# Optimization experiments

Hardware: AMD Instinct MI355X
Metric: run time of the kernel (lower is better)

Reference implementation:

```python
import jax, jax.numpy as jnp
import numpy as np

B, C, IMG, P_SZ = 32, 3, 224, 16
NPATCH = (IMG // P_SZ) ** 2  # 196
D, H, LAYERS, MLP = 768, 12, 12, 3072
HD = D // H
POOL, SEL, PLEN, NCLS = 10, 5, 5, 100
LN_EPS = 1e-6


def layer_norm(x, w, b):
    m = jnp.mean(x, -1, keepdims=True)
    v = jnp.var(x, -1, keepdims=True)
    return (x - m) * jax.lax.rsqrt(v + LN_EPS) * w + b


def vit_blocks(x, stacked):
    def blk(x, p):
        l1w, l1b, qw, qb, pw, pb, l2w, l2b, f1w, f1b, f2w, f2b = p
        b, s, _ = x.shape
        h = layer_norm(x, l1w, l1b)
        qkv = (h @ qw + qb).reshape(b, s, 3, H, HD).transpose(2, 0, 3, 1, 4)
        q, k, v = qkv[0], qkv[1], qkv[2]
        att = jax.nn.softmax(jnp.einsum('bhqd,bhkd->bhqk', q, k) * (HD ** -0.5), axis=-1)
        o = jnp.einsum('bhqk,bhkd->bhqd', att, v).transpose(0, 2, 1, 3).reshape(b, s, D)
        x = x + o @ pw + pb
        h = layer_norm(x, l2w, l2b)
        x = x + jax.nn.gelu(h @ f1w + f1b, approximate=False) @ f2w + f2b
        return x, None
    return jax.lax.scan(blk, x, stacked)[0]


def forward(inputs, patch_w, patch_b, cls_token, pos_embed,
            ln1_w, ln1_b, qkv_w, qkv_b, proj_w, proj_b,
            ln2_w, ln2_b, fc1_w, fc1_b, fc2_w, fc2_b,
            norm_w, norm_b, head_w, head_b,
            key_pool, frequency, prompts, variance, inv_variance):
    b = inputs.shape[0]
    g = IMG // P_SZ
    # patchify: 16x16/s16 conv == linear over [C,ph,pw]-flattened patches
    patches = inputs.reshape(b, C, g, P_SZ, g, P_SZ).transpose(0, 2, 4, 1, 3, 5).reshape(b, NPATCH, C * P_SZ * P_SZ)
    x = patches @ patch_w + patch_b  # [B,196,D]
    t = jnp.concatenate([jnp.broadcast_to(cls_token, (b, 1, D)), x], axis=1)
    x = t + pos_embed  # [B,197,D]
    stacked = (ln1_w, ln1_b, qkv_w, qkv_b, proj_w, proj_b, ln2_w, ln2_b, fc1_w, fc1_b, fc2_w, fc2_b)
    q = vit_blocks(x, stacked)
    q = layer_norm(q, norm_w, norm_b)[:, 0]  # CLS query [B,D]
    # Mahalanobis routing. torch computes exp(-quad/2)*(2pi)^{D/2}*||var||_F^{1/2},
    # which overflows fp32; we rank in log-domain (monotone-identical, constant
    # (D/2)log(2pi) dropped), so topk indices match the intended math.
    diff = q[:, None, :] - jax.lax.stop_gradient(key_pool)  # [B,POOL,D]
    quad = jnp.einsum('bpd,pde,bpe->bp', diff, inv_variance, diff)
    lognorm = 0.5 * jnp.log(jnp.linalg.norm(variance.reshape(POOL, -1), axis=-1))
    logprob = -0.5 * quad + lognorm
    w = frequency.max() - frequency  # F.normalize(...)
    wn = w / jnp.maximum(jnp.linalg.norm(w), 1e-12)
    score = logprob + jnp.log(jnp.maximum(wn, 1e-30))
    _, topk = jax.lax.top_k(-score, SEL)  # smallest SEL, ascending by score
    p = prompts[topk].reshape(b, SEL * PLEN, D) + pos_embed[0, 0]
    sx = jnp.concatenate([x[:, :1], p, x[:, 1:]], axis=1)  # [B,222,D]
    sx = vit_blocks(sx, stacked)
    sx = layer_norm(sx, norm_w, norm_b)
    feat = sx[:, 1:SEL * PLEN + 1].mean(axis=1)
    return feat @ head_w + head_b


def setup_inputs():
    key = jax.random.key(0)
    ks = jax.random.split(key, 16)
    std = 0.02
    inp = {
        'inputs': jax.random.normal(ks[0], (B, C, IMG, IMG), jnp.float32),
        'patch_w': jax.random.normal(ks[1], (C * P_SZ * P_SZ, D)) * std,
        'patch_b': jnp.zeros((D,)),
        'cls_token': jax.random.normal(ks[2], (1, 1, D)) * std,
        'pos_embed': jax.random.normal(ks[3], (1, NPATCH + 1, D)) * std,
        'ln1_w': jnp.ones((LAYERS, D)), 'ln1_b': jnp.zeros((LAYERS, D)),
        'qkv_w': jax.random.normal(ks[4], (LAYERS, D, 3 * D)) * std,
        'qkv_b': jnp.zeros((LAYERS, 3 * D)),
        'proj_w': jax.random.normal(ks[5], (LAYERS, D, D)) * std,
        'proj_b': jnp.zeros((LAYERS, D)),
        'ln2_w': jnp.ones((LAYERS, D)), 'ln2_b': jnp.zeros((LAYERS, D)),
        'fc1_w': jax.random.normal(ks[6], (LAYERS, D, MLP)) * std,
        'fc1_b': jnp.zeros((LAYERS, MLP)),
        'fc2_w': jax.random.normal(ks[7], (LAYERS, MLP, D)) * std,
        'fc2_b': jnp.zeros((LAYERS, D)),
        'norm_w': jnp.ones((D,)), 'norm_b': jnp.zeros((D,)),
        'head_w': jax.random.normal(ks[8], (D, NCLS)) * std,
        'head_b': jnp.zeros((NCLS,)),
        'key_pool': jax.random.normal(ks[9], (POOL, D)),
        'frequency': jax.random.randint(ks[10], (POOL,), 1, 100).astype(jnp.float32),
        'prompts': jax.random.normal(ks[11], (POOL, PLEN, D)) * std,
    }
    a = jax.random.uniform(ks[12], (POOL, D, D)) * 2.0
    var = a + jnp.swapaxes(a, -1, -2)  # symmetric, as in __init__
    inp['variance'] = var
    inp['inv_variance'] = jnp.linalg.inv(var)
    return inp


reference = forward
```

## Files before the change

kernel.cpp:

```cpp
#include <hip/hip_runtime.h>
#include <math.h>

#define S_PAD  224
#define NTOK   7168
#define DM     768
#define NH     12
#define HDIM   64
#define DMLP   3072
#define NBATCH 32
#define NLAYER 12
#define NPOOL  10
#define NSEL   5
#define NPLEN  5
#define NCLS   100
#define LN_EPS 1e-6f

typedef _Float16 f16_t;
typedef _Float16 f16x8 __attribute__((ext_vector_type(8)));
typedef float    floatx4 __attribute__((ext_vector_type(4)));

__device__ inline void cp16_lds(void* lds, const void* gp) {
    __builtin_amdgcn_global_load_lds((const __attribute__((address_space(1))) void*)gp,
                                     (__attribute__((address_space(3))) void*)lds, 16, 0, 0);
}

__global__ void wconv_t(const float* __restrict__ W, f16_t* __restrict__ WT, int K, int N) {
    int layer = blockIdx.z;
    const float* Wp = W + (long)layer * K * N;
    f16_t* Tp = WT + (long)layer * K * N;
    __shared__ float tile[32][33];
    int n0 = blockIdx.x * 32, k0 = blockIdx.y * 32;
    int tc = threadIdx.x & 31, tr = threadIdx.x >> 5;
    #pragma unroll
    for (int rr = 0; rr < 32; rr += 8)
        tile[tr + rr][tc] = Wp[(long)(k0 + tr + rr) * N + n0 + tc];
    __syncthreads();
    #pragma unroll
    for (int rr = 0; rr < 32; rr += 8)
        Tp[(long)(n0 + tr + rr) * K + k0 + tc] = (f16_t)tile[tc][tr + rr];
}

__global__ void patchify(const float* __restrict__ inp, f16_t* __restrict__ PATCH) {
    int s = blockIdx.x, b = blockIdx.y, t = threadIdx.x;
    f16_t* dst = PATCH + ((long)b * S_PAD + s) * DM;
    if (s >= 196) { for (int e = t; e < DM; e += 256) dst[e] = (f16_t)0.0f; return; }
    int py = s / 14, px = s % 14;
    for (int e = t; e < DM; e += 256) {
        int c = e >> 8, ph = (e >> 4) & 15, pw = e & 15;
        dst[e] = (f16_t)inp[(((long)b * 3 + c) * 224 + py * 16 + ph) * 224 + px * 16 + pw];
    }
}

template<int EPI, int BM>
__global__ __launch_bounds__(256) void gemm_f16(
    const f16_t* __restrict__ A, const f16_t* __restrict__ Bt,
    const float* __restrict__ bias, const float* __restrict__ resid,
    float* __restrict__ outf, f16_t* __restrict__ outb, int N, int K)
{
    constexpr int MI = BM / 32;
    __shared__ __align__(16) f16_t ldsA[BM * 32];
    __shared__ __align__(16) f16_t ldsB[128 * 32];
    const int t = threadIdx.x;
    const int w = t >> 6, l = t & 63;
    const int lr = l & 15, quad = l >> 4;
    const long m0 = (long)blockIdx.x * BM, n0 = (long)blockIdx.y * 128;
    const int r = t >> 2, c8 = (t & 3) << 3;
    const f16_t* Ap = A + (m0 + (r % BM)) * (long)K + c8;
    const f16_t* Bp = Bt + (n0 + r) * (long)K + c8;
    const int wm = (w >> 1) * (BM >> 1), wn = (w & 1) << 6;
    char* lbA = (char*)ldsA + (w << 10);
    char* lbB = (char*)ldsB + (w << 10);
    floatx4 acc[MI][4];
    #pragma unroll
    for (int i = 0; i < MI; i++)
        #pragma unroll
        for (int j = 0; j < 4; j++) acc[i][j] = (floatx4){0.f, 0.f, 0.f, 0.f};

    for (int k0 = 0; k0 < K; k0 += 32) {
        __syncthreads();
        cp16_lds(lbA, Ap + k0);
        if (BM == 128) cp16_lds(lbA + 4096, Ap + (long)64 * K + k0);
        cp16_lds(lbB,        Bp + k0);
        cp16_lds(lbB + 4096, Bp + (long)64 * K + k0);
        __syncthreads();
        f16x8 af[MI], bf[4];
        #pragma unroll
        for (int mi = 0; mi < MI; mi++)
            af[mi] = *(const f16x8*)((const char*)ldsA + ((wm + mi * 16 + lr) << 6) + (quad << 4));
        #pragma unroll
        for (int ni = 0; ni < 4; ni++)
            bf[ni] = *(const f16x8*)((const char*)ldsB + ((wn + ni * 16 + lr) << 6) + (quad << 4));
        #pragma unroll
        for (int mi = 0; mi < MI; mi++)
            #pragma unroll
            for (int ni = 0; ni < 4; ni++)
                acc[mi][ni] = __builtin_amdgcn_mfma_f32_16x16x32_f16(af[mi], bf[ni], acc[mi][ni], 0, 0, 0);
    }
    #pragma unroll
    for (int mi = 0; mi < MI; mi++) {
        const long row = m0 + wm + mi * 16 + quad * 4;
        #pragma unroll
        for (int ni = 0; ni < 4; ni++) {
            const long col = n0 + wn + ni * 16 + lr;
            const float bv = bias[col];
            #pragma unroll
            for (int rg = 0; rg < 4; rg++) {
                long idx = (row + rg) * (long)N + col;
                float v = acc[mi][ni][rg] + bv;
                if (EPI == 0) outf[idx] = v;
                else if (EPI == 1) outb[idx] = (f16_t)v;
                else if (EPI == 2) outf[idx] = v + resid[idx];
                else {
                    v = 0.5f * v * (1.0f + erff(v * 0.70710678118654752f));
                    outb[idx] = (f16_t)v;
                }
            }
        }
    }
}

__global__ void assemble_x0(const float* __restrict__ PE, const float* __restrict__ cls,
                            const float* __restrict__ pos, float* __restrict__ X0,
                            float* __restrict__ X) {
    int s = blockIdx.x, b = blockIdx.y, t = threadIdx.x;
    long o = ((long)b * S_PAD + s) * DM;
    for (int e = t; e < DM; e += 256) {
        float v;
        if (s == 0)        v = cls[e] + pos[e];
        else if (s <= 196) v = PE[((long)b * S_PAD + (s - 1)) * DM + e] + pos[(long)s * DM + e];
        else               v = 0.0f;
        X0[o + e] = v; X[o + e] = v;
    }
}

__global__ __launch_bounds__(256) void ln_to_f16(const float* __restrict__ X,
        const float* __restrict__ gw, const float* __restrict__ gb, f16_t* __restrict__ out) {
    const long row = blockIdx.x;
    const int t = threadIdx.x;
    const float* x = X + row * DM;
    float v0 = x[t], v1 = x[t + 256], v2 = x[t + 512];
    float s = v0 + v1 + v2, ss = v0 * v0 + v1 * v1 + v2 * v2;
    #pragma unroll
    for (int off = 32; off; off >>= 1) { s += __shfl_down(s, off); ss += __shfl_down(ss, off); }
    __shared__ float sa[8];
    int w = t >> 6;
    if ((t & 63) == 0) { sa[w] = s; sa[4 + w] = ss; }
    __syncthreads();
    s = sa[0] + sa[1] + sa[2] + sa[3]; ss = sa[4] + sa[5] + sa[6] + sa[7];
    float mean = s * (1.0f / DM);
    float var = ss * (1.0f / DM) - mean * mean;
    float rs = rsqrtf(var + LN_EPS);
    f16_t* o = out + row * DM;
    o[t]       = (f16_t)((v0 - mean) * rs * gw[t]       + gb[t]);
    o[t + 256] = (f16_t)((v1 - mean) * rs * gw[t + 256] + gb[t + 256]);
    o[t + 512] = (f16_t)((v2 - mean) * rs * gw[t + 512] + gb[t + 512]);
}

__global__ __launch_bounds__(256) void v_trans(const f16_t* __restrict__ qkv,
                                               f16_t* __restrict__ vtg) {
    int bh = blockIdx.x, b = bh / NH, h = bh % NH;
    __shared__ __align__(16) char lds[32768];
    int t = threadIdx.x, w = t >> 6, l = t & 63;
    const f16_t* Vb = qkv + (long)b * S_PAD * 2304 + 1536 + h * HDIM;
    #pragma unroll
    for (int q = 0; q < 8; q++) {
        int c0 = q * 256 + w * 64;
        int cc = c0 + l;
        int j = cc / 9, part = cc - j * 9;
        if (j > 223) j = 223;
        if (part > 7) part = 7;
        cp16_lds(lds + (size_t)c0 * 16, Vb + (long)j * 2304 + part * 8);
    }
    __syncthreads();
    const f16_t* Vs = (const f16_t*)lds;
    f16_t* dst = vtg + (long)bh * HDIM * S_PAD;
    #pragma unroll
    for (int it = 0; it < 56; it++) {
        int e = it * 256 + t;
        int d = e / S_PAD, j = e - d * S_PAD;
        dst[e] = Vs[j * 72 + d];
    }
}

__global__ __launch_bounds__(256) void attn_fused(const f16_t* __restrict__ qkv,
        const f16_t* __restrict__ vtg, f16_t* __restrict__ AO, int S) {
    int bh = blockIdx.y, b = bh / NH, h = bh % NH;
    int i0 = blockIdx.x * 64;
    int t = threadIdx.x, w = t >> 6, l = t & 63;
    int lr = l & 15, quad = l >> 4;
    __shared__ __align__(16) char lds[62464];
    const f16_t* Kb = qkv + (long)b * S_PAD * 2304 + 768 + h * HDIM;
    const f16_t* Qb = qkv + (long)b * S_PAD * 2304 + h * HDIM;
    const f16_t* Vg = vtg + (long)bh * HDIM * S_PAD;

    #pragma unroll
    for (int q = 0; q < 8; q++) {
        int c0 = q * 256 + w * 64;
        int cc = c0 + l;
        int j = cc / 9, part = cc - j * 9;
        if (j > 223) j = 223;
        if (part > 7) part = 7;
        cp16_lds(lds + (size_t)c0 * 16, Kb + (long)j * 2304 + part * 8);
    }
    #pragma unroll
    for (int q = 0; q < 8; q++) {
        int c0 = q * 256 + w * 64;
        if (c0 < 1856) {
            int cc = c0 + l;
            int d = cc / 29, part = cc - d * 29;
            if (part > 27) part = 27;
            cp16_lds(lds + 32768 + (size_t)c0 * 16, Vg + (long)d * S_PAD + part * 8);
        }
    }
    int qr = i0 + w * 16 + lr;
    if (qr > S_PAD - 1) qr = S_PAD - 1;
    long qrow = (long)qr * 2304;
    f16x8 qf0 = *(const f16x8*)(Qb + qrow + quad * 8);
    f16x8 qf1 = *(const f16x8*)(Qb + qrow + 32 + quad * 8);
    __syncthreads();

    const f16_t* Ks = (const f16_t*)lds;
    floatx4 acc[14];
    #pragma unroll
    for (int jt = 0; jt < 14; jt++) {
        floatx4 a = (floatx4){0.f, 0.f, 0.f, 0.f};
        f16x8 k0 = *(const f16x8*)(Ks + (jt * 16 + lr) * 72 + quad * 8);
        f16x8 k1 = *(const f16x8*)(Ks + (jt * 16 + lr) * 72 + 32 + quad * 8);
        a = __builtin_amdgcn_mfma_f32_16x16x32_f16(qf0, k0, a, 0, 0, 0);
        a = __builtin_amdgcn_mfma_f32_16x16x32_f16(qf1, k1, a, 0, 0, 0);
        acc[jt] = a;
    }
    float mx[4] = {-3.0e38f, -3.0e38f, -3.0e38f, -3.0e38f};
    #pragma unroll
    for (int jt = 0; jt < 14; jt++) {
        bool valid = (jt * 16 + lr) < S;
        #pragma unroll
        for (int rg = 0; rg < 4; rg++) {
            float v = valid ? acc[jt][rg] * 0.125f : -3.0e38f;
            acc[jt][rg] = v;
            mx[rg] = fmaxf(mx[rg], v);
        }
    }
    #pragma unroll
    for (int rg = 0; rg < 4; rg++)
        #pragma unroll
        for (int m = 1; m < 16; m <<= 1) mx[rg] = fmaxf(mx[rg], __shfl_xor(mx[rg], m));
    float sm[4] = {0.f, 0.f, 0.f, 0.f};
    #pragma unroll
    for (int jt = 0; jt < 14; jt++)
        #pragma unroll
        for (int rg = 0; rg < 4; rg++) {
            float e = __expf(acc[jt][rg] - mx[rg]);
            acc[jt][rg] = e; sm[rg] += e;
        }
    #pragma unroll
    for (int rg = 0; rg < 4; rg++)
        #pragma unroll
        for (int m = 1; m < 16; m <<= 1) sm[rg] += __shfl_xor(sm[rg], m);

    __syncthreads();
    f16_t* Pw = (f16_t*)lds + w * 16 * 232;
    #pragma unroll
    for (int jt = 0; jt < 14; jt++)
        #pragma unroll
        for (int rg = 0; rg < 4; rg++)
            Pw[(quad * 4 + rg) * 232 + jt * 16 + lr] = (f16_t)acc[jt][rg];

    const f16_t* Vt = (const f16_t*)(lds + 32768);
    floatx4 oacc[4];
    #pragma unroll
    for (int dt = 0; dt < 4; dt++) oacc[dt] = (floatx4){0.f, 0.f, 0.f, 0.f};
    #pragma unroll
    for (int ks = 0; ks < 7; ks++) {
        f16x8 a = *(const f16x8*)(Pw + lr * 232 + ks * 32 + quad * 8);
        #pragma unroll
        for (int dt = 0; dt < 4; dt++) {
            f16x8 bb = *(const f16x8*)(Vt + (dt * 16 + lr) * 232 + ks * 32 + quad * 8);
            oacc[dt] = __builtin_amdgcn_mfma_f32_16x16x32_f16(a, bb, oacc[dt], 0, 0, 0);
        }
    }
    if (i0 + w * 16 < S_PAD) {
        float inv[4];
        #pragma unroll
        for (int rg = 0; rg < 4; rg++) inv[rg] = 1.0f / sm[rg];
        f16_t* dst = AO + (long)b * S_PAD * DM + h * HDIM;
        #pragma unroll
        for (int dt = 0; dt < 4; dt++)
            #pragma unroll
            for (int rg = 0; rg < 4; rg++)
                dst[(long)(i0 + w * 16 + quad * 4 + rg) * DM + dt * 16 + lr] = (f16_t)(oacc[dt][rg] * inv[rg]);
    }
}

__global__ void cls_ln(const float* __restrict__ X, const float* __restrict__ gw,
                       const float* __restrict__ gb, float* __restrict__ q) {
    int b = blockIdx.x, t = threadIdx.x;
    const float* x = X + (long)b * S_PAD * DM;
    float v0 = x[t], v1 = x[t + 256], v2 = x[t + 512];
    float s = v0 + v1 + v2, ss = v0 * v0 + v1 * v1 + v2 * v2;
    #pragma unroll
    for (int off = 32; off; off >>= 1) { s += __shfl_down(s, off); ss += __shfl_down(ss, off); }
    __shared__ float sa[8];
    int w = t >> 6;
    if ((t & 63) == 0) { sa[w] = s; sa[4 + w] = ss; }
    __syncthreads();
    s = sa[0] + sa[1] + sa[2] + sa[3]; ss = sa[4] + sa[5] + sa[6] + sa[7];
    float mean = s * (1.0f / DM);
    float rs = rsqrtf(ss * (1.0f / DM) - mean * mean + LN_EPS);
    q[(long)b * DM + t]       = (v0 - mean) * rs * gw[t]       + gb[t];
    q[(long)b * DM + t + 256] = (v1 - mean) * rs * gw[t + 256] + gb[t + 256];
    q[(long)b * DM + t + 512] = (v2 - mean) * rs * gw[t + 512] + gb[t + 512];
}

__global__ void var_ssq(const float* __restrict__ var, float* __restrict__ ssq) {
    int p = blockIdx.x, chunk = blockIdx.y;
    const float* v = var + (long)p * DM * DM + (long)chunk * 16384;
    float s = 0.f;
    for (int i = threadIdx.x; i < 16384; i += 256) { float x = v[i]; s += x * x; }
    #pragma unroll
    for (int off = 32; off; off >>= 1) s += __shfl_down(s, off);
    __shared__ float sa[4];
    int w = threadIdx.x >> 6;
    if ((threadIdx.x & 63) == 0) sa[w] = s;
    __syncthreads();
    if (threadIdx.x == 0) atomicAdd(&ssq[p], sa[0] + sa[1] + sa[2] + sa[3]);
}

__global__ void route_coef(const float* __restrict__ ssq, const float* __restrict__ freq,
                           float* __restrict__ coef) {
    if (threadIdx.x == 0) {
        float fm = freq[0];
        for (int p = 1; p < NPOOL; p++) fm = fmaxf(fm, freq[p]);
        float w[NPOOL]; float n2 = 0.f;
        for (int p = 0; p < NPOOL; p++) { w[p] = fm - freq[p]; n2 += w[p] * w[p]; }
        float nrm = fmaxf(sqrtf(n2), 1e-12f);
        for (int p = 0; p < NPOOL; p++) {
            float wn = w[p] / nrm;
            coef[p] = 0.25f * logf(ssq[p]) + logf(fmaxf(wn, 1e-30f));
        }
    }
}

__global__ __launch_bounds__(256) void route_quad(const float* __restrict__ q,
        const float* __restrict__ kp, const float* __restrict__ iv,
        const float* __restrict__ coef, float* __restrict__ score) {
    int b = blockIdx.x, p = blockIdx.y, t = threadIdx.x;
    __shared__ float diff[DM];
    for (int e = t; e < DM; e += 256) diff[e] = q[(long)b * DM + e] - kp[(long)p * DM + e];
    __syncthreads();
    const float* M = iv + (long)p * DM * DM;
    float u0 = 0.f, u1 = 0.f, u2 = 0.f;
    for (int i = 0; i < DM; i++) {
        float di = diff[i];
        const float* r = M + (long)i * DM;
        u0 += di * r[t]; u1 += di * r[t + 256]; u2 += di * r[t + 512];
    }
    float part = u0 * diff[t] + u1 * diff[t + 256] + u2 * diff[t + 512];
    #pragma unroll
    for (int off = 32; off; off >>= 1) part += __shfl_down(part, off);
    __shared__ float sa[4];
    if ((t & 63) == 0) sa[t >> 6] = part;
    __syncthreads();
    if (t == 0) score[b * NPOOL + p] = -0.5f * (sa[0] + sa[1] + sa[2] + sa[3]) + coef[p];
}

__global__ void topk_kernel(const float* __restrict__ score, int* __restrict__ topk) {
    int b = threadIdx.x;
    if (b < NBATCH) {
        float s[NPOOL]; bool used[NPOOL];
        for (int p = 0; p < NPOOL; p++) { s[p] = score[b * NPOOL + p]; used[p] = false; }
        for (int k = 0; k < NSEL; k++) {
            int best = 0; float bv = 3.4e38f;
            for (int p = 0; p < NPOOL; p++)
                if (!used[p] && s[p] < bv) { bv = s[p]; best = p; }
            used[best] = true; topk[b * NSEL + k] = best;
        }
    }
}

__global__ void assemble_sx(const float* __restrict__ X0, const float* __restrict__ prompts,
                            const float* __restrict__ pos, const int* __restrict__ topk,
                            float* __restrict__ X) {
    int s = blockIdx.x, b = blockIdx.y, t = threadIdx.x;
    long o = ((long)b * S_PAD + s) * DM;
    for (int e = t; e < DM; e += 256) {
        float v;
        if (s == 0) v = X0[(long)b * S_PAD * DM + e];
        else if (s <= 25) {
            int j = s - 1;
            int pr = topk[b * NSEL + j / NPLEN];
            v = prompts[((long)pr * NPLEN + j % NPLEN) * DM + e] + pos[e];
        } else if (s <= 221) {
            v = X0[((long)b * S_PAD + (s - 25)) * DM + e];
        } else v = 0.0f;
        X[o + e] = v;
    }
}

__global__ __launch_bounds__(256) void feat_ln_mean(const float* __restrict__ X,
        const float* __restrict__ gw, const float* __restrict__ gb, float* __restrict__ feat) {
    int b = blockIdx.x, t = threadIdx.x;
    __shared__ float sa[8];
    float f0 = 0.f, f1 = 0.f, f2 = 0.f;
    for (int j = 1; j <= NSEL * NPLEN; j++) {
        const float* x = X + ((long)b * S_PAD + j) * DM;
        float v0 = x[t], v1 = x[t + 256], v2 = x[t + 512];
        float s = v0 + v1 + v2, ss = v0 * v0 + v1 * v1 + v2 * v2;
        #pragma unroll
        for (int off = 32; off; off >>= 1) { s += __shfl_down(s, off); ss += __shfl_down(ss, off); }
        __syncthreads();
        int w = t >> 6;
        if ((t & 63) == 0) { sa[w] = s; sa[4 + w] = ss; }
        __syncthreads();
        s = sa[0] + sa[1] + sa[2] + sa[3]; ss = sa[4] + sa[5] + sa[6] + sa[7];
        float mean = s * (1.0f / DM);
        float rs = rsqrtf(ss * (1.0f / DM) - mean * mean + LN_EPS);
        f0 += (v0 - mean) * rs; f1 += (v1 - mean) * rs; f2 += (v2 - mean) * rs;
    }
    const float k = 1.0f / (NSEL * NPLEN);
    feat[(long)b * DM + t]       = f0 * k * gw[t]       + gb[t];
    feat[(long)b * DM + t + 256] = f1 * k * gw[t + 256] + gb[t + 256];
    feat[(long)b * DM + t + 512] = f2 * k * gw[t + 512] + gb[t + 512];
}

__global__ void head_gemm(const float* __restrict__ feat, const float* __restrict__ hw,
                          const float* __restrict__ hb, float* __restrict__ out) {
    int b = blockIdx.x, c = threadIdx.x;
    if (c < NCLS) {
        float a = hb[c];
        const float* f = feat + (long)b * DM;
        for (int k = 0; k < DM; k++) a += f[k] * hw[(long)k * NCLS + c];
        out[b * NCLS + c] = a;
    }
}

extern "C" void kernel_launch(void* const* d_in, const int* in_sizes, int n_in,
                              void* d_out, int out_size, void* d_ws, size_t ws_size,
                              hipStream_t stream) {
    const float* inputs   = (const float*)d_in[0];
    const float* patch_w  = (const float*)d_in[1];
    const float* patch_b  = (const float*)d_in[2];
    const float* cls_tok  = (const float*)d_in[3];
    const float* pos_emb  = (const float*)d_in[4];
    const float* ln1_w    = (const float*)d_in[5];
    const float* ln1_b    = (const float*)d_in[6];
    const float* qkv_w    = (const float*)d_in[7];
    const float* qkv_b    = (const float*)d_in[8];
    const float* proj_w   = (const float*)d_in[9];
    const float* proj_b   = (const float*)d_in[10];
    const float* ln2_w    = (const float*)d_in[11];
    const float* ln2_b    = (const float*)d_in[12];
    const float* fc1_w    = (const float*)d_in[13];
    const float* fc1_b    = (const float*)d_in[14];
    const float* fc2_w    = (const float*)d_in[15];
    const float* fc2_b    = (const float*)d_in[16];
    const float* norm_w   = (const float*)d_in[17];
    const float* norm_b   = (const float*)d_in[18];
    const float* head_w   = (const float*)d_in[19];
    const float* head_b   = (const float*)d_in[20];
    const float* key_pool = (const float*)d_in[21];
    const float* freq     = (const float*)d_in[22];
    const float* prompts  = (const float*)d_in[23];
    const float* variance = (const float*)d_in[24];
    const float* inv_var  = (const float*)d_in[25];
    float* out = (float*)d_out;

    char* p = (char*)d_ws;
    auto alloc = [&](size_t bytes) { char* r = p; p += (bytes + 255) & ~(size_t)255; return r; };
    f16_t* WTpatch = (f16_t*)alloc(768UL * 768 * 2);
    f16_t* WTq  = (f16_t*)alloc(12UL * 2304 * 768 * 2);
    f16_t* WTpr = (f16_t*)alloc(12UL * 768 * 768 * 2);
    f16_t* WTf1 = (f16_t*)alloc(12UL * 3072 * 768 * 2);
    f16_t* WTf2 = (f16_t*)alloc(12UL * 768 * 3072 * 2);
    float*  X    = (float*)alloc((size_t)NTOK * DM * 4);
    float*  X0   = (float*)alloc((size_t)NTOK * DM * 4);
    f16_t* Hb   = (f16_t*)alloc((size_t)NTOK * DM * 2);
    f16_t* QKV  = (f16_t*)alloc((size_t)NTOK * 2304 * 2);
    f16_t* VTg  = (f16_t*)alloc(384UL * HDIM * S_PAD * 2);
    f16_t* AO   = (f16_t*)alloc((size_t)NTOK * DM * 2);
    char* RSC    = alloc(384UL * S_PAD * S_PAD * 4);
    char* RP     = alloc(384UL * S_PAD * S_PAD * 2);
    float* qv    = (float*)alloc(NBATCH * DM * 4);
    float* feat  = (float*)alloc(NBATCH * DM * 4);
    float* ssq   = (float*)alloc(NPOOL * 4);
    float* coef  = (float*)alloc(NPOOL * 4);
    float* score = (float*)alloc(NBATCH * NPOOL * 4);
    int*   tki   = (int*)alloc(NBATCH * NSEL * 4);
    f16_t* MID  = (f16_t*)RSC;
    float*  PE   = (float*)RSC;
    f16_t* PATCH= (f16_t*)RP;

    wconv_t<<<dim3(768/32, 768/32, 1), 256, 0, stream>>>(patch_w, WTpatch, 768, 768);
    wconv_t<<<dim3(2304/32, 768/32, 12), 256, 0, stream>>>(qkv_w, WTq, 768, 2304);
    wconv_t<<<dim3(768/32, 768/32, 12), 256, 0, stream>>>(proj_w, WTpr, 768, 768);
    wconv_t<<<dim3(3072/32, 768/32, 12), 256, 0, stream>>>(fc1_w, WTf1, 768, 3072);
    wconv_t<<<dim3(768/32, 3072/32, 12), 256, 0, stream>>>(fc2_w, WTf2, 3072, 768);

    patchify<<<dim3(S_PAD, NBATCH), 256, 0, stream>>>(inputs, PATCH);
    gemm_f16<0,64><<<dim3(112, 6), 256, 0, stream>>>(PATCH, WTpatch, patch_b, nullptr, PE, nullptr, 768, 768);
    assemble_x0<<<dim3(S_PAD, NBATCH), 256, 0, stream>>>(PE, cls_tok, pos_emb, X0, X);

    auto run_layers = [&](int S) {
        for (int l = 0; l < NLAYER; l++) {
            ln_to_f16<<<NTOK, 256, 0, stream>>>(X, ln1_w + l * DM, ln1_b + l * DM, Hb);
            gemm_f16<1,128><<<dim3(56, 18), 256, 0, stream>>>(Hb, WTq + (long)l * 2304 * 768,
                qkv_b + l * 2304, nullptr, nullptr, QKV, 2304, 768);
            v_trans<<<384, 256, 0, stream>>>(QKV, VTg);
            attn_fused<<<dim3(4, 384), 256, 0, stream>>>(QKV, VTg, AO, S);
            gemm_f16<2,64><<<dim3(112, 6), 256, 0, stream>>>(AO, WTpr + (long)l * 768 * 768,
                proj_b + l * DM, X, X, nullptr, 768, 768);
            ln_to_f16<<<NTOK, 256, 0, stream>>>(X, ln2_w + l * DM, ln2_b + l * DM, Hb);
            gemm_f16<3,128><<<dim3(56, 24), 256, 0, stream>>>(Hb, WTf1 + (long)l * 3072 * 768,
                fc1_b + l * DMLP, nullptr, nullptr, MID, 3072, 768);
            gemm_f16<2,64><<<dim3(112, 6), 256, 0, stream>>>(MID, WTf2 + (long)l * 768 * 3072,
                fc2_b + l * DM, X, X, nullptr, 768, 3072);
        }
    };

    run_layers(197);

    cls_ln<<<NBATCH, 256, 0, stream>>>(X, norm_w, norm_b, qv);
    hipMemsetAsync(ssq, 0, NPOOL * 4, stream);
    var_ssq<<<dim3(NPOOL, 36), 256, 0, stream>>>(variance, ssq);
    route_coef<<<1, 64, 0, stream>>>(ssq, freq, coef);
    route_quad<<<dim3(NBATCH, NPOOL), 256, 0, stream>>>(qv, key_pool, inv_var, coef, score);
    topk_kernel<<<1, 32, 0, stream>>>(score, tki);
    assemble_sx<<<dim3(S_PAD, NBATCH), 256, 0, stream>>>(X0, prompts, pos_emb, tki, X);

    run_layers(222);

    feat_ln_mean<<<NBATCH, 256, 0, stream>>>(X, norm_w, norm_b, feat);
    head_gemm<<<NBATCH, 128, 0, stream>>>(feat, head_w, head_b, out);
    (void)in_sizes; (void)n_in; (void)out_size; (void)ws_size;
}
```

Baseline: 7.006 ms.

## Swizzle GEMM LDS layout and use 64x64 tiles for N=768 GEMMs

Adds an XOR-style rotation of the 16-byte chunk position within each 64-byte LDS row, applied both to the global-to-LDS copy and to the fragment reads, so that MFMA operand loads spread across banks instead of conflicting. It also adds a BN template parameter and switches the proj, fc2 and patch GEMMs (N=768) to 64x64 tiles with twice as many blocks, which improves CU occupancy and wave count on the many-CU GPU. The cost is less data reuse per block and more redundant A loads for the smaller tiles.

Measured after the change: 7.326 ms. 1.05x slower.

```diff
diff --git a/kernel.cpp b/kernel.cpp
--- a/kernel.cpp
+++ b/kernel.cpp
@@ -51,56 +51,68 @@
     }
 }
 
-template<int EPI, int BM>
+template<int EPI, int BM, int BN>
 __global__ __launch_bounds__(256) void gemm_f16(
     const f16_t* __restrict__ A, const f16_t* __restrict__ Bt,
     const float* __restrict__ bias, const float* __restrict__ resid,
     float* __restrict__ outf, f16_t* __restrict__ outb, int N, int K)
 {
-    constexpr int MI = BM / 32;
+    constexpr int MI = BM / 32, NI = BN / 32;
     __shared__ __align__(16) f16_t ldsA[BM * 32];
-    __shared__ __align__(16) f16_t ldsB[128 * 32];
+    __shared__ __align__(16) f16_t ldsB[BN * 32];
     const int t = threadIdx.x;
     const int w = t >> 6, l = t & 63;
     const int lr = l & 15, quad = l >> 4;
-    const long m0 = (long)blockIdx.x * BM, n0 = (long)blockIdx.y * 128;
-    const int r = t >> 2, c8 = (t & 3) << 3;
-    const f16_t* Ap = A + (m0 + (r % BM)) * (long)K + c8;
+    const long m0 = (long)blockIdx.x * BM, n0 = (long)blockIdx.y * BN;
+    const int r = t >> 2;
+    const int c8 = (((t & 3) - (t >> 3)) & 3) << 3;
+    const f16_t* Ap = A + (m0 + r) * (long)K + c8;
     const f16_t* Bp = Bt + (n0 + r) * (long)K + c8;
-    const int wm = (w >> 1) * (BM >> 1), wn = (w & 1) << 6;
+    const int wm = (w >> 1) * (BM / 2), wn = (w & 1) * (BN / 2);
     char* lbA = (char*)ldsA + (w << 10);
     char* lbB = (char*)ldsB + (w << 10);
-    floatx4 acc[MI][4];
+    int aoff[MI], boff[NI];
+    #pragma unroll
+    for (int mi = 0; mi < MI; mi++) {
+        int R = wm + mi * 16 + lr;
+        aoff[mi] = (R << 6) + (((quad + (R >> 1)) & 3) << 4);
+    }
+    #pragma unroll
+    for (int ni = 0; ni < NI; ni++) {
+        int R = wn + ni * 16 + lr;
+        boff[ni] = (R << 6) + (((quad + (R >> 1)) & 3) << 4);
+    }
+    floatx4 acc[MI][NI];
     #pragma unroll
     for (int i = 0; i < MI; i++)
         #pragma unroll
-        for (int j = 0; j < 4; j++) acc[i][j] = (floatx4){0.f, 0.f, 0.f, 0.f};
+        for (int j = 0; j < NI; j++) acc[i][j] = (floatx4){0.f, 0.f, 0.f, 0.f};
 
     for (int k0 = 0; k0 < K; k0 += 32) {
         __syncthreads();
         cp16_lds(lbA, Ap + k0);
-        if (BM == 128) cp16_lds(lbA + 4096, Ap + (long)64 * K + k0);
-        cp16_lds(lbB,        Bp + k0);
-        cp16_lds(lbB + 4096, Bp + (long)64 * K + k0);
+        if constexpr (BM == 128) cp16_lds(lbA + 4096, Ap + (long)64 * K + k0);
+        cp16_lds(lbB, Bp + k0);
+        if constexpr (BN == 128) cp16_lds(lbB + 4096, Bp + (long)64 * K + k0);
         __syncthreads();
-        f16x8 af[MI], bf[4];
+        f16x8 af[MI], bf[NI];
         #pragma unroll
         for (int mi = 0; mi < MI; mi++)
-            af[mi] = *(const f16x8*)((const char*)ldsA + ((wm + mi * 16 + lr) << 6) + (quad << 4));
-        #pragma unroll
-        for (int ni = 0; ni < 4; ni++)
-            bf[ni] = *(const f16x8*)((const char*)ldsB + ((wn + ni * 16 + lr) << 6) + (quad << 4));
+            af[mi] = *(const f16x8*)((const char*)ldsA + aoff[mi]);
+        #pragma unroll
+        for (int ni = 0; ni < NI; ni++)
+            bf[ni] = *(const f16x8*)((const char*)ldsB + boff[ni]);
         #pragma unroll
         for (int mi = 0; mi < MI; mi++)
             #pragma unroll
-            for (int ni = 0; ni < 4; ni++)
+            for (int ni = 0; ni < NI; ni++)
                 acc[mi][ni] = __builtin_amdgcn_mfma_f32_16x16x32_f16(af[mi], bf[ni], acc[mi][ni], 0, 0, 0);
     }
     #pragma unroll
     for (int mi = 0; mi < MI; mi++) {
         const long row = m0 + wm + mi * 16 + quad * 4;
         #pragma unroll
-        for (int ni = 0; ni < 4; ni++) {
+        for (int ni = 0; ni < NI; ni++) {
             const long col = n0 + wn + ni * 16 + lr;
             const float bv = bias[col];
             #pragma unroll
@@ -497,22 +509,22 @@
     wconv_t<<<dim3(768/32, 3072/32, 12), 256, 0, stream>>>(fc2_w, WTf2, 3072, 768);
 
     patchify<<<dim3(S_PAD, NBATCH), 256, 0, stream>>>(inputs, PATCH);
-    gemm_f16<0,64><<<dim3(112, 6), 256, 0, stream>>>(PATCH, WTpatch, patch_b, nullptr, PE, nullptr, 768, 768);
+    gemm_f16<0,64,64><<<dim3(112, 12), 256, 0, stream>>>(PATCH, WTpatch, patch_b, nullptr, PE, nullptr, 768, 768);
     assemble_x0<<<dim3(S_PAD, NBATCH), 256, 0, stream>>>(PE, cls_tok, pos_emb, X0, X);
 
     auto run_layers = [&](int S) {
         for (int l = 0; l < NLAYER; l++) {
             ln_to_f16<<<NTOK, 256, 0, stream>>>(X, ln1_w + l * DM, ln1_b + l * DM, Hb);
-            gemm_f16<1,128><<<dim3(56, 18), 256, 0, stream>>>(Hb, WTq + (long)l * 2304 * 768,
+            gemm_f16<1,128,128><<<dim3(56, 18), 256, 0, stream>>>(Hb, WTq + (long)l * 2304 * 768,
                 qkv_b + l * 2304, nullptr, nullptr, QKV, 2304, 768);
             v_trans<<<384, 256, 0, stream>>>(QKV, VTg);
             attn_fused<<<dim3(4, 384), 256, 0, stream>>>(QKV, VTg, AO, S);
-            gemm_f16<2,64><<<dim3(112, 6), 256, 0, stream>>>(AO, WTpr + (long)l * 768 * 768,
+            gemm_f16<2,64,64><<<dim3(112, 12), 256, 0, stream>>>(AO, WTpr + (long)l * 768 * 768,
                 proj_b + l * DM, X, X, nullptr, 768, 768);
             ln_to_f16<<<NTOK, 256, 0, stream>>>(X, ln2_w + l * DM, ln2_b + l * DM, Hb);
-            gemm_f16<3,128><<<dim3(56, 24), 256, 0, stream>>>(Hb, WTf1 + (long)l * 3072 * 768,
+            gemm_f16<3,128,128><<<dim3(56, 24), 256, 0, stream>>>(Hb, WTf1 + (long)l * 3072 * 768,
                 fc1_b + l * DMLP, nullptr, nullptr, MID, 3072, 768);
-            gemm_f16<2,64><<<dim3(112, 6), 256, 0, stream>>>(MID, WTf2 + (long)l * 768 * 3072,
+            gemm_f16<2,64,64><<<dim3(112, 12), 256, 0, stream>>>(MID, WTf2 + (long)l * 768 * 3072,
                 fc2_b + l * DM, X, X, nullptr, 768, 3072);
         }
     };
```
